# Kernel tuning notes

Hardware: AMD Instinct MI355X
Metric: run time of the kernel (lower is better)

Reference implementation:

```python
import jax, jax.numpy as jnp
import numpy as np

K = 10  # num_neighbors in original nn_index call


def setup_inputs() -> dict:
    key = jax.random.key(0)
    k1, k2, k3, k4 = jax.random.split(key, 4)
    B, OBS, ACT, N = 256, 32, 2, 500000
    obs = jax.random.normal(k1, (B, OBS), dtype=jnp.float32)
    action = jax.random.normal(k2, (B, ACT), dtype=jnp.float32)
    mem_sa = jax.random.normal(k3, (N, OBS + ACT), dtype=jnp.float32)
    mem_Q = jax.random.normal(k4, (N, 1), dtype=jnp.float32)
    return {"obs": obs, "action": action, "mem_sa": mem_sa, "mem_Q": mem_Q}


def reference(obs, action, mem_sa, mem_Q):
    # query: [B, D] state-action, brute-force kNN over memory table [N, D]
    q = jnp.concatenate([obs, action], axis=1)
    # squared Euclidean distances (FLANN returns squared L2): [B, N]
    d2 = (jnp.sum(q * q, axis=1, keepdims=True)
          - 2.0 * q @ mem_sa.T
          + jnp.sum(mem_sa * mem_sa, axis=1)[None, :])
    neg_d, idx = jax.lax.top_k(-d2, K)   # nearest K neighbors
    dists = -neg_d                        # [B, K], ascending
    Qs = mem_Q[idx, 0]                    # gather Q values: [B, K]
    # NOTE: original applies softmax to raw distances (not negated)
    weights = jax.nn.softmax(dists, axis=1)
    return jnp.sum(weights * Qs, axis=1)  # [B]
```

## Files before the change

### kernel.cpp

```cpp
#include <hip/hip_runtime.h>
#include <hip/hip_bf16.h>
#include <math.h>

#define NPTS   500000
#define NB     256
#define TOPK   10
#define CAP    2048
#define SBLK   1024
#define SPER   16
#define MARGIN 2.0f
#define NWCH   15625
#define FBLK   1536
#define LCAP   8
#define PMAIN  393216
#define OCAP   32768

typedef short v2s  __attribute__((ext_vector_type(2)));
typedef short v4s  __attribute__((ext_vector_type(4)));
typedef short v8s  __attribute__((ext_vector_type(8)));
typedef float v16f __attribute__((ext_vector_type(16)));

__device__ __forceinline__ unsigned short f2bf(float f) {
    unsigned u = __float_as_uint(f);
    unsigned r = u + 0x7FFFu + ((u >> 16) & 1u);
    return (unsigned short)(r >> 16);
}
__device__ __forceinline__ float bf2f(unsigned short h) {
    return __uint_as_float(((unsigned)h) << 16);
}
__device__ __forceinline__ v2s pk2(float2 f) {
    __hip_bfloat162 h = __float22bfloat162_rn(f);
    v2s r;
    __builtin_memcpy(&r, &h, 4);
    return r;
}

__device__ __forceinline__ float norm34(const float* __restrict__ r) {
    float a0 = 0.f, a1 = 0.f, a2 = 0.f, a3 = 0.f;
#pragma unroll
    for (int d = 0; d < 32; d += 4) {
        a0 = fmaf(r[d + 0], r[d + 0], a0);
        a1 = fmaf(r[d + 1], r[d + 1], a1);
        a2 = fmaf(r[d + 2], r[d + 2], a2);
        a3 = fmaf(r[d + 3], r[d + 3], a3);
    }
    a0 = fmaf(r[32], r[32], a0);
    a1 = fmaf(r[33], r[33], a1);
    return (a0 + a1) + (a2 + a3);
}
__device__ __forceinline__ float dot34(const float* __restrict__ r, const float* q) {
    float a0 = 0.f, a1 = 0.f, a2 = 0.f, a3 = 0.f;
#pragma unroll
    for (int d = 0; d < 32; d += 4) {
        a0 = fmaf(r[d + 0], q[d + 0], a0);
        a1 = fmaf(r[d + 1], q[d + 1], a1);
        a2 = fmaf(r[d + 2], q[d + 2], a2);
        a3 = fmaf(r[d + 3], q[d + 3], a3);
    }
    a0 = fmaf(r[32], q[32], a0);
    a1 = fmaf(r[33], q[33], a1);
    return (a0 + a1) + (a2 + a3);
}
__device__ __forceinline__ float dot34_v4(const float4* __restrict__ r4, const float* q) {
    float a0 = 0.f, a1 = 0.f, a2 = 0.f, a3 = 0.f;
#pragma unroll
    for (int dp = 0; dp < 8; ++dp) {
        float4 v = r4[dp];
        a0 = fmaf(v.x, q[4 * dp + 0], a0);
        a1 = fmaf(v.y, q[4 * dp + 1], a1);
        a2 = fmaf(v.z, q[4 * dp + 2], a2);
        a3 = fmaf(v.w, q[4 * dp + 3], a3);
    }
    float2 t = *(const float2*)(r4 + 8);
    a0 = fmaf(t.x, q[32], a0);
    a1 = fmaf(t.y, q[33], a1);
    return (a0 + a1) + (a2 + a3);
}
__device__ __forceinline__ void load_q(const float* __restrict__ obs,
                                       const float* __restrict__ act, int b, float* q) {
#pragma unroll
    for (int d = 0; d < 32; ++d) q[d] = obs[b * 32 + d];
    q[32] = act[b * 2 + 0];
    q[33] = act[b * 2 + 1];
}

__global__ __launch_bounds__(256, 4) void k_sample(const float* __restrict__ obs,
                                                   const float* __restrict__ act,
                                                   const float* __restrict__ msa,
                                                   float* __restrict__ minima) {
    __shared__ __align__(16) float sm[SPER * 36];
    __shared__ float smn[SPER];
    const int g = blockIdx.x, t = threadIdx.x;
    const int base = g * SPER;
    for (int i = t; i < SPER * 34; i += 256) {
        int row = i / 34, d = i - row * 34;
        sm[row * 36 + d] = msa[(size_t)base * 34 + i];
    }
    __syncthreads();
    if (t < SPER) smn[t] = norm34(&sm[t * 36]);
    __syncthreads();
    float q[34];
    load_q(obs, act, t, q);
    float best = __builtin_inff();
#pragma unroll
    for (int j = 0; j < SPER; ++j) {
        float s = fmaf(-2.f, dot34_v4((const float4*)&sm[j * 36], q), smn[j]);
        best = fminf(best, s);
    }
    minima[(size_t)t * SBLK + g] = best;
}

__global__ __launch_bounds__(64) void k_tau(const float* __restrict__ minima,
                                            const float* __restrict__ obs,
                                            const float* __restrict__ act,
                                            v8s* __restrict__ afrag,
                                            int* __restrict__ cursor) {
    __shared__ __align__(16) unsigned short qs[48];
    const int b = blockIdx.x, lane = threadIdx.x;
    if (b == 0 && lane == 0) { cursor[0] = 0; cursor[1] = 0; }
    float v[16];
#pragma unroll
    for (int k = 0; k < 16; ++k) v[k] = minima[(size_t)b * SBLK + lane + 64 * k];
    float last = 0.f;
    for (int r = 0; r < TOPK; ++r) {
        float lm = v[0]; int la = 0;
#pragma unroll
        for (int k = 1; k < 16; ++k) { if (v[k] < lm) { lm = v[k]; la = k; } }
        float wm = lm;
        for (int off = 32; off; off >>= 1) wm = fminf(wm, __shfl_xor(wm, off));
        unsigned long long msk = __ballot(lm == wm);
        int first = (int)__builtin_ctzll(msk);
        if (lane == first) {
#pragma unroll
            for (int k = 0; k < 16; ++k) { if (k == la) v[k] = __builtin_inff(); }
        }
        last = wm;
    }
    float val = 0.f;
    if (lane < 32)       val = obs[b * 32 + lane];
    else if (lane < 34)  val = act[b * 2 + (lane - 32)];
    else if (lane == 34) val = -0.5f;
    else if (lane == 35) val = 0.5f * (last + MARGIN);
    if (lane < 48) qs[lane] = (lane < 36) ? f2bf(val) : (unsigned short)0;
    __syncthreads();
    if (lane < 6) {
        int s = lane >> 1, half = lane & 1;
        int qt = b >> 5, mrow = b & 31;
        v8s frag = *(const v8s*)&qs[s * 16 + half * 8];
        afrag[(qt * 3 + s) * 64 + half * 32 + mrow] = frag;
    }
}

__global__ __launch_bounds__(256, 3) void k_filter(const float* __restrict__ msa,
                                                   const v8s* __restrict__ afrag,
                                                   int* __restrict__ cursor,
                                                   unsigned* __restrict__ pbuf,
                                                   int* __restrict__ posq) {
    __shared__ int lcount[NB];
    __shared__ int lcand[NB * LCAP];
    __shared__ int gbase;
    const int g = blockIdx.x, t = threadIdx.x;
    const int w = t >> 6, lane = t & 63;
    const int mrow = lane & 31, half = lane >> 5;
    lcount[t] = 0;
    __syncthreads();
    v8s A[8][3];
#pragma unroll
    for (int qt = 0; qt < 8; ++qt)
#pragma unroll
        for (int s = 0; s < 3; ++s)
            A[qt][s] = afrag[(qt * 3 + s) * 64 + lane];
    const v16f zacc = (v16f)0.0f;
    const int gw = g * 4 + w;
#pragma unroll 1
    for (int wc = gw; wc < NWCH; wc += FBLK * 4) {
        const int p0 = wc * 32 + mrow;
        const float* rp = msa + (size_t)p0 * 34;
        float2 e0 = *(const float2*)(rp + half * 8 + 0);
        float2 e1 = *(const float2*)(rp + half * 8 + 2);
        float2 e2 = *(const float2*)(rp + half * 8 + 4);
        float2 e3 = *(const float2*)(rp + half * 8 + 6);
        float2 e4 = *(const float2*)(rp + 16 + half * 8 + 0);
        float2 e5 = *(const float2*)(rp + 16 + half * 8 + 2);
        float2 e6 = *(const float2*)(rp + 16 + half * 8 + 4);
        float2 e7 = *(const float2*)(rp + 16 + half * 8 + 6);
        float2 e8 = *(const float2*)(rp + 32);
        float n0 = 0.f, n1 = 0.f;
        n0 = fmaf(e0.x, e0.x, n0); n1 = fmaf(e0.y, e0.y, n1);
        n0 = fmaf(e1.x, e1.x, n0); n1 = fmaf(e1.y, e1.y, n1);
        n0 = fmaf(e2.x, e2.x, n0); n1 = fmaf(e2.y, e2.y, n1);
        n0 = fmaf(e3.x, e3.x, n0); n1 = fmaf(e3.y, e3.y, n1);
        n0 = fmaf(e4.x, e4.x, n0); n1 = fmaf(e4.y, e4.y, n1);
        n0 = fmaf(e5.x, e5.x, n0); n1 = fmaf(e5.y, e5.y, n1);
        n0 = fmaf(e6.x, e6.x, n0); n1 = fmaf(e6.y, e6.y, n1);
        n0 = fmaf(e7.x, e7.x, n0); n1 = fmaf(e7.y, e7.y, n1);
        float part = n0 + n1;
        part = fmaf(e8.x, e8.x * 0.5f, part);
        part = fmaf(e8.y, e8.y * 0.5f, part);
        float nrm = part + __shfl_xor(part, 32);
        float thr = 0.5f * nrm;
        v4s b0lo = __builtin_shufflevector(pk2(e0), pk2(e1), 0, 1, 2, 3);
        v4s b0hi = __builtin_shufflevector(pk2(e2), pk2(e3), 0, 1, 2, 3);
        v8s B0 = __builtin_shufflevector(b0lo, b0hi, 0, 1, 2, 3, 4, 5, 6, 7);
        v4s b1lo = __builtin_shufflevector(pk2(e4), pk2(e5), 0, 1, 2, 3);
        v4s b1hi = __builtin_shufflevector(pk2(e6), pk2(e7), 0, 1, 2, 3);
        v8s B1 = __builtin_shufflevector(b1lo, b1hi, 0, 1, 2, 3, 4, 5, 6, 7);
        v8s B2 = (v8s)(short)0;
        if (half == 0) {
            v2s m33 = pk2(e8);
            B2[0] = m33[0];
            B2[1] = m33[1];
            B2[3] = (short)0x3F80;
        }
#pragma unroll
        for (int qt = 0; qt < 8; ++qt) {
            v16f acc = __builtin_amdgcn_mfma_f32_32x32x16_bf16(A[qt][0], B0, zacc, 0, 0, 0);
            acc = __builtin_amdgcn_mfma_f32_32x32x16_bf16(A[qt][1], B1, acc, 0, 0, 0);
            acc = __builtin_amdgcn_mfma_f32_32x32x16_bf16(A[qt][2], B2, acc, 0, 0, 0);
            unsigned hm = 0;
#pragma unroll
            for (int r = 0; r < 16; ++r) hm |= (acc[r] >= thr) ? (1u << r) : 0u;
            while (hm) {
                int r = __builtin_ctz(hm);
                hm &= hm - 1;
                int qq = qt * 32 + (r & 3) + 8 * (r >> 2) + 4 * half;
                int slot = atomicAdd(&lcount[qq], 1);
                if (slot < LCAP) lcand[qq * LCAP + slot] = p0;
                else {
                    int dg = atomicAdd(cursor + 1, 1);
                    if (dg < OCAP) pbuf[PMAIN + dg] = ((unsigned)qq << 19) | (unsigned)p0;
                }
            }
        }
    }
    __syncthreads();
    int n = lcount[t];
    if (n > LCAP) n = LCAP;
    lcount[t] = n;
    __syncthreads();
    for (int off = 1; off < 256; off <<= 1) {
        int v = (t >= off) ? lcount[t - off] : 0;
        __syncthreads();
        lcount[t] += v;
        __syncthreads();
    }
    int base_l = lcount[t] - n;
    if (t == 255) gbase = atomicAdd(cursor, lcount[255]);
    __syncthreads();
    int start = gbase + base_l;
    if (start >= PMAIN) { start = 0; n = 0; }
    else if (start + n > PMAIN) n = PMAIN - start;
    posq[g * NB + t] = start | (n << 20);
    for (int i = 0; i < n; ++i)
        pbuf[start + i] = (unsigned)lcand[t * LCAP + i];
}

__global__ __launch_bounds__(256) void k_final(const float* __restrict__ obs,
                                               const float* __restrict__ act,
                                               const float* __restrict__ msa,
                                               const unsigned* __restrict__ pbuf,
                                               const int* __restrict__ posq,
                                               const int* __restrict__ cursor,
                                               const float* __restrict__ memQ,
                                               float* __restrict__ out) {
    __shared__ float ls[CAP];
    __shared__ int   li[CAP];
    __shared__ int   sc[NB];
    __shared__ int   lcnt;
    __shared__ float rs[4];
    __shared__ int   ri[4];
    __shared__ float sel_s[TOPK];
    __shared__ int   sel_i[TOPK];
    const int b = blockIdx.x, t = threadIdx.x;
    const int lane = t & 63, wid = t >> 6;
    int nk[6], pk6[6], tot = 0;
#pragma unroll
    for (int k = 0; k < 6; ++k) {
        int packed = posq[(size_t)(t + 256 * k) * NB + b];
        nk[k] = (packed >> 20) & 0xF;
        pk6[k] = packed & 0xFFFFF;
        tot += nk[k];
    }
    sc[t] = tot;
    __syncthreads();
    for (int off = 1; off < 256; off <<= 1) {
        int v = (t >= off) ? sc[t - off] : 0;
        __syncthreads();
        sc[t] += v;
        __syncthreads();
    }
    int myoff = sc[t] - tot;
    if (t == 0) lcnt = (sc[255] > CAP) ? CAP : sc[255];
    __syncthreads();
#pragma unroll
    for (int k = 0; k < 6; ++k)
        for (int i = 0; i < nk[k]; ++i) {
            if (myoff < CAP) li[myoff] = (int)pbuf[pk6[k] + i];
            ++myoff;
        }
    int novf = cursor[1];
    if (novf > OCAP) novf = OCAP;
    for (int j = t; j < novf; j += 256) {
        unsigned pr = pbuf[PMAIN + j];
        if ((int)(pr >> 19) == b) {
            int s = atomicAdd(&lcnt, 1);
            if (s < CAP) li[s] = (int)(pr & 0x7FFFFu);
        }
    }
    __syncthreads();
    int cnt = lcnt;
    if (cnt > CAP) cnt = CAP;
    float q[34];
    load_q(obs, act, b, q);
    for (int j = t; j < cnt; j += 256) {
        const float* row = msa + (size_t)li[j] * 34;
        ls[j] = fmaf(-2.f, dot34(row, q), norm34(row));
    }
    __syncthreads();
    for (int k = 0; k < TOPK; ++k) {
        float bs = __builtin_inff();
        int   bi = 0x7fffffff;
        for (int j = t; j < cnt; j += 256) {
            float s = ls[j]; int i = li[j];
            if (s < bs || (s == bs && i < bi)) { bs = s; bi = i; }
        }
        for (int off = 32; off; off >>= 1) {
            float s2 = __shfl_down(bs, off);
            int   i2 = __shfl_down(bi, off);
            if (s2 < bs || (s2 == bs && i2 < bi)) { bs = s2; bi = i2; }
        }
        if (lane == 0) { rs[wid] = bs; ri[wid] = bi; }
        __syncthreads();
        if (t == 0) {
            float fs = rs[0]; int fi = ri[0];
#pragma unroll
            for (int ww = 1; ww < 4; ++ww) {
                if (rs[ww] < fs || (rs[ww] == fs && ri[ww] < fi)) { fs = rs[ww]; fi = ri[ww]; }
            }
            sel_s[k] = fs; sel_i[k] = fi;
        }
        __syncthreads();
        const int win = sel_i[k];
        for (int j = t; j < cnt; j += 256) {
            if (li[j] == win) ls[j] = __builtin_inff();
        }
        __syncthreads();
    }
    if (t == 0) {
        float m = sel_s[TOPK - 1];
        float wsum = 0.f, acc = 0.f;
#pragma unroll
        for (int k = 0; k < TOPK; ++k) {
            if (sel_i[k] == 0x7fffffff) continue;
            float w2 = expf(sel_s[k] - m);
            wsum += w2;
            acc = fmaf(w2, memQ[sel_i[k]], acc);
        }
        out[b] = acc / wsum;
    }
}

extern "C" void kernel_launch(void* const* d_in, const int* in_sizes, int n_in,
                              void* d_out, int out_size, void* d_ws, size_t ws_size,
                              hipStream_t stream) {
    const float* obs = (const float*)d_in[0];
    const float* act = (const float*)d_in[1];
    const float* msa = (const float*)d_in[2];
    const float* mq  = (const float*)d_in[3];
    float* out = (float*)d_out;

    char* ws = (char*)d_ws;
    int*      cursor = (int*)ws;
    v8s*      afrag  = (v8s*)(ws + 256);
    float*    minima = (float*)(ws + 32768);
    int*      posq   = (int*)(ws + 32768 + 1048576);
    unsigned* pbuf   = (unsigned*)(ws + 32768 + 1048576 + 1572864);

    k_sample<<<SBLK, 256, 0, stream>>>(obs, act, msa, minima);
    k_tau   <<<NB, 64, 0, stream>>>(minima, obs, act, afrag, cursor);
    k_filter<<<FBLK, 256, 0, stream>>>(msa, afrag, cursor, pbuf, posq);
    k_final <<<NB, 256, 0, stream>>>(obs, act, msa, pbuf, posq, cursor, mq, out);
}
```

Measured before the change: 174.9 us.

## Prefetch next memory rows in filter loop, cut filter grid, add max early-out

The filter kernel now software-pipelines its global loads, fetching the next chunk's rows into registers while MFMA and thresholding run on the current chunk. The grid shrinks from 1536 to 512 blocks, with launch bounds lowered to 2 waves per SIMD to make room for the extra registers, and the final kernel scans correspondingly fewer per-block segments. Each MFMA tile also gets a max-reduce early-out, so the per-row bitmask and atomics are skipped when no entry passes the threshold. The trade is more register pressure and lower occupancy in exchange for hidden load latency and less divergent per-tile work.

```diff
diff --git a/kernel.cpp b/kernel.cpp
--- a/kernel.cpp
+++ b/kernel.cpp
@@ -10,7 +10,8 @@
 #define SPER   16
 #define MARGIN 2.0f
 #define NWCH   15625
-#define FBLK   1536
+#define FBLK   512
+#define NSEG   2
 #define LCAP   8
 #define PMAIN  393216
 #define OCAP   32768
@@ -82,6 +83,18 @@
     for (int d = 0; d < 32; ++d) q[d] = obs[b * 32 + d];
     q[32] = act[b * 2 + 0];
     q[33] = act[b * 2 + 1];
+}
+__device__ __forceinline__ void load9(float2* __restrict__ e,
+                                      const float* __restrict__ rp, int half) {
+    e[0] = *(const float2*)(rp + half * 8 + 0);
+    e[1] = *(const float2*)(rp + half * 8 + 2);
+    e[2] = *(const float2*)(rp + half * 8 + 4);
+    e[3] = *(const float2*)(rp + half * 8 + 6);
+    e[4] = *(const float2*)(rp + 16 + half * 8 + 0);
+    e[5] = *(const float2*)(rp + 16 + half * 8 + 2);
+    e[6] = *(const float2*)(rp + 16 + half * 8 + 4);
+    e[7] = *(const float2*)(rp + 16 + half * 8 + 6);
+    e[8] = *(const float2*)(rp + 32);
 }
 
 __global__ __launch_bounds__(256, 4) void k_sample(const float* __restrict__ obs,
@@ -151,7 +164,7 @@
     }
 }
 
-__global__ __launch_bounds__(256, 3) void k_filter(const float* __restrict__ msa,
+__global__ __launch_bounds__(256, 2) void k_filter(const float* __restrict__ msa,
                                                    const v8s* __restrict__ afrag,
                                                    int* __restrict__ cursor,
                                                    unsigned* __restrict__ pbuf,
@@ -162,52 +175,49 @@
     const int g = blockIdx.x, t = threadIdx.x;
     const int w = t >> 6, lane = t & 63;
     const int mrow = lane & 31, half = lane >> 5;
-    lcount[t] = 0;
-    __syncthreads();
     v8s A[8][3];
 #pragma unroll
     for (int qt = 0; qt < 8; ++qt)
 #pragma unroll
         for (int s = 0; s < 3; ++s)
             A[qt][s] = afrag[(qt * 3 + s) * 64 + lane];
+    lcount[t] = 0;
+    __syncthreads();
     const v16f zacc = (v16f)0.0f;
     const int gw = g * 4 + w;
+    const int step = FBLK * 4;
+    float2 c[9], nx[9];
+    int wc = gw;
+    load9(c, msa + (size_t)(wc * 32 + mrow) * 34, half);
 #pragma unroll 1
-    for (int wc = gw; wc < NWCH; wc += FBLK * 4) {
+    for (; wc < NWCH; ) {
+        const int wn = wc + step;
+        const int pn = (wn < NWCH) ? wn : gw;
+        load9(nx, msa + (size_t)(pn * 32 + mrow) * 34, half);
         const int p0 = wc * 32 + mrow;
-        const float* rp = msa + (size_t)p0 * 34;
-        float2 e0 = *(const float2*)(rp + half * 8 + 0);
-        float2 e1 = *(const float2*)(rp + half * 8 + 2);
-        float2 e2 = *(const float2*)(rp + half * 8 + 4);
-        float2 e3 = *(const float2*)(rp + half * 8 + 6);
-        float2 e4 = *(const float2*)(rp + 16 + half * 8 + 0);
-        float2 e5 = *(const float2*)(rp + 16 + half * 8 + 2);
-        float2 e6 = *(const float2*)(rp + 16 + half * 8 + 4);
-        float2 e7 = *(const float2*)(rp + 16 + half * 8 + 6);
-        float2 e8 = *(const float2*)(rp + 32);
         float n0 = 0.f, n1 = 0.f;
-        n0 = fmaf(e0.x, e0.x, n0); n1 = fmaf(e0.y, e0.y, n1);
-        n0 = fmaf(e1.x, e1.x, n0); n1 = fmaf(e1.y, e1.y, n1);
-        n0 = fmaf(e2.x, e2.x, n0); n1 = fmaf(e2.y, e2.y, n1);
-        n0 = fmaf(e3.x, e3.x, n0); n1 = fmaf(e3.y, e3.y, n1);
-        n0 = fmaf(e4.x, e4.x, n0); n1 = fmaf(e4.y, e4.y, n1);
-        n0 = fmaf(e5.x, e5.x, n0); n1 = fmaf(e5.y, e5.y, n1);
-        n0 = fmaf(e6.x, e6.x, n0); n1 = fmaf(e6.y, e6.y, n1);
-        n0 = fmaf(e7.x, e7.x, n0); n1 = fmaf(e7.y, e7.y, n1);
+        n0 = fmaf(c[0].x, c[0].x, n0); n1 = fmaf(c[0].y, c[0].y, n1);
+        n0 = fmaf(c[1].x, c[1].x, n0); n1 = fmaf(c[1].y, c[1].y, n1);
+        n0 = fmaf(c[2].x, c[2].x, n0); n1 = fmaf(c[2].y, c[2].y, n1);
+        n0 = fmaf(c[3].x, c[3].x, n0); n1 = fmaf(c[3].y, c[3].y, n1);
+        n0 = fmaf(c[4].x, c[4].x, n0); n1 = fmaf(c[4].y, c[4].y, n1);
+        n0 = fmaf(c[5].x, c[5].x, n0); n1 = fmaf(c[5].y, c[5].y, n1);
+        n0 = fmaf(c[6].x, c[6].x, n0); n1 = fmaf(c[6].y, c[6].y, n1);
+        n0 = fmaf(c[7].x, c[7].x, n0); n1 = fmaf(c[7].y, c[7].y, n1);
         float part = n0 + n1;
-        part = fmaf(e8.x, e8.x * 0.5f, part);
-        part = fmaf(e8.y, e8.y * 0.5f, part);
+        part = fmaf(c[8].x, c[8].x * 0.5f, part);
+        part = fmaf(c[8].y, c[8].y * 0.5f, part);
         float nrm = part + __shfl_xor(part, 32);
         float thr = 0.5f * nrm;
-        v4s b0lo = __builtin_shufflevector(pk2(e0), pk2(e1), 0, 1, 2, 3);
-        v4s b0hi = __builtin_shufflevector(pk2(e2), pk2(e3), 0, 1, 2, 3);
+        v4s b0lo = __builtin_shufflevector(pk2(c[0]), pk2(c[1]), 0, 1, 2, 3);
+        v4s b0hi = __builtin_shufflevector(pk2(c[2]), pk2(c[3]), 0, 1, 2, 3);
         v8s B0 = __builtin_shufflevector(b0lo, b0hi, 0, 1, 2, 3, 4, 5, 6, 7);
-        v4s b1lo = __builtin_shufflevector(pk2(e4), pk2(e5), 0, 1, 2, 3);
-        v4s b1hi = __builtin_shufflevector(pk2(e6), pk2(e7), 0, 1, 2, 3);
+        v4s b1lo = __builtin_shufflevector(pk2(c[4]), pk2(c[5]), 0, 1, 2, 3);
+        v4s b1hi = __builtin_shufflevector(pk2(c[6]), pk2(c[7]), 0, 1, 2, 3);
         v8s B1 = __builtin_shufflevector(b1lo, b1hi, 0, 1, 2, 3, 4, 5, 6, 7);
         v8s B2 = (v8s)(short)0;
         if (half == 0) {
-            v2s m33 = pk2(e8);
+            v2s m33 = pk2(c[8]);
             B2[0] = m33[0];
             B2[1] = m33[1];
             B2[3] = (short)0x3F80;
@@ -217,21 +227,32 @@
             v16f acc = __builtin_amdgcn_mfma_f32_32x32x16_bf16(A[qt][0], B0, zacc, 0, 0, 0);
             acc = __builtin_amdgcn_mfma_f32_32x32x16_bf16(A[qt][1], B1, acc, 0, 0, 0);
             acc = __builtin_amdgcn_mfma_f32_32x32x16_bf16(A[qt][2], B2, acc, 0, 0, 0);
-            unsigned hm = 0;
-#pragma unroll
-            for (int r = 0; r < 16; ++r) hm |= (acc[r] >= thr) ? (1u << r) : 0u;
-            while (hm) {
-                int r = __builtin_ctz(hm);
-                hm &= hm - 1;
-                int qq = qt * 32 + (r & 3) + 8 * (r >> 2) + 4 * half;
-                int slot = atomicAdd(&lcount[qq], 1);
-                if (slot < LCAP) lcand[qq * LCAP + slot] = p0;
-                else {
-                    int dg = atomicAdd(cursor + 1, 1);
-                    if (dg < OCAP) pbuf[PMAIN + dg] = ((unsigned)qq << 19) | (unsigned)p0;
+            float m01 = fmaxf(acc[0], acc[1]),   m23 = fmaxf(acc[2], acc[3]);
+            float m45 = fmaxf(acc[4], acc[5]),   m67 = fmaxf(acc[6], acc[7]);
+            float m89 = fmaxf(acc[8], acc[9]),   mab = fmaxf(acc[10], acc[11]);
+            float mcd = fmaxf(acc[12], acc[13]), mef = fmaxf(acc[14], acc[15]);
+            float mx = fmaxf(fmaxf(fmaxf(m01, m23), fmaxf(m45, m67)),
+                             fmaxf(fmaxf(m89, mab), fmaxf(mcd, mef)));
+            if (mx >= thr) {
+                unsigned hm = 0;
+#pragma unroll
+                for (int r = 0; r < 16; ++r) hm |= (acc[r] >= thr) ? (1u << r) : 0u;
+                while (hm) {
+                    int r = __builtin_ctz(hm);
+                    hm &= hm - 1;
+                    int qq = qt * 32 + (r & 3) + 8 * (r >> 2) + 4 * half;
+                    int slot = atomicAdd(&lcount[qq], 1);
+                    if (slot < LCAP) lcand[qq * LCAP + slot] = p0;
+                    else {
+                        int dg = atomicAdd(cursor + 1, 1);
+                        if (dg < OCAP) pbuf[PMAIN + dg] = ((unsigned)qq << 19) | (unsigned)p0;
+                    }
                 }
             }
         }
+#pragma unroll
+        for (int i = 0; i < 9; ++i) c[i] = nx[i];
+        wc = wn;
     }
     __syncthreads();
     int n = lcount[t];
@@ -273,9 +294,9 @@
     __shared__ int   sel_i[TOPK];
     const int b = blockIdx.x, t = threadIdx.x;
     const int lane = t & 63, wid = t >> 6;
-    int nk[6], pk6[6], tot = 0;
-#pragma unroll
-    for (int k = 0; k < 6; ++k) {
+    int nk[NSEG], pk6[NSEG], tot = 0;
+#pragma unroll
+    for (int k = 0; k < NSEG; ++k) {
         int packed = posq[(size_t)(t + 256 * k) * NB + b];
         nk[k] = (packed >> 20) & 0xF;
         pk6[k] = packed & 0xFFFFF;
@@ -293,7 +314,7 @@
     if (t == 0) lcnt = (sc[255] > CAP) ? CAP : sc[255];
     __syncthreads();
 #pragma unroll
-    for (int k = 0; k < 6; ++k)
+    for (int k = 0; k < NSEG; ++k)
         for (int i = 0; i < nk[k]; ++i) {
             if (myoff < CAP) li[myoff] = (int)pbuf[pk6[k] + i];
             ++myoff;
```

Result: faster. 171.3 us (-2.1%).

## Stage memory chunks through double-buffered LDS and split query tiles across waves

Applied to the files above, without the earlier changes.

The filter kernel now loads each 32-point chunk of the memory table cooperatively into a double-buffered shared-memory tile, prefetching the next chunk while the current one is processed. Each of the four waves handles two of the eight query tiles for the same chunk, so each wave holds fewer A fragments and occupancy rises. A cheap max-reduction skips building the hit mask when no accumulator passes the threshold. The block count drops to 1024, and the final kernel reads 4 position segments instead of 6 to match. The trade-off is an added __syncthreads per chunk and 4 waves each recomputing norms and bf16 packing for the same points.

```diff
diff --git a/kernel.cpp b/kernel.cpp
--- a/kernel.cpp
+++ b/kernel.cpp
@@ -10,10 +10,12 @@
 #define SPER   16
 #define MARGIN 2.0f
 #define NWCH   15625
-#define FBLK   1536
+#define FBLK   1024
+#define NSEG   4
 #define LCAP   8
 #define PMAIN  393216
 #define OCAP   32768
+#define CHB    4352
 
 typedef short v2s  __attribute__((ext_vector_type(2)));
 typedef short v4s  __attribute__((ext_vector_type(4)));
@@ -151,31 +153,41 @@
     }
 }
 
-__global__ __launch_bounds__(256, 3) void k_filter(const float* __restrict__ msa,
+__global__ __launch_bounds__(256, 4) void k_filter(const float* __restrict__ msa,
                                                    const v8s* __restrict__ afrag,
                                                    int* __restrict__ cursor,
                                                    unsigned* __restrict__ pbuf,
                                                    int* __restrict__ posq) {
+    __shared__ __align__(16) float chunk[2][CHB / 4];
     __shared__ int lcount[NB];
     __shared__ int lcand[NB * LCAP];
     __shared__ int gbase;
     const int g = blockIdx.x, t = threadIdx.x;
     const int w = t >> 6, lane = t & 63;
     const int mrow = lane & 31, half = lane >> 5;
+    v8s A[2][3];
+#pragma unroll
+    for (int j = 0; j < 2; ++j)
+#pragma unroll
+        for (int s = 0; s < 3; ++s)
+            A[j][s] = afrag[((w * 2 + j) * 3 + s) * 64 + lane];
     lcount[t] = 0;
-    __syncthreads();
-    v8s A[8][3];
-#pragma unroll
-    for (int qt = 0; qt < 8; ++qt)
-#pragma unroll
-        for (int s = 0; s < 3; ++s)
-            A[qt][s] = afrag[(qt * 3 + s) * 64 + lane];
     const v16f zacc = (v16f)0.0f;
-    const int gw = g * 4 + w;
-#pragma unroll 1
-    for (int wc = gw; wc < NWCH; wc += FBLK * 4) {
-        const int p0 = wc * 32 + mrow;
-        const float* rp = msa + (size_t)p0 * 34;
+
+    float4 sreg; float treg = 0.f;
+    const char* mb = (const char*)msa;
+    auto stage_load = [&](int c) {
+        const char* cb = mb + (size_t)c * CHB;
+        sreg = *(const float4*)(cb + t * 16);
+        if (t < 64) treg = *(const float*)(cb + 4096 + t * 4);
+    };
+    auto stage_write = [&](int nb) {
+        *(float4*)((char*)&chunk[nb][0] + t * 16) = sreg;
+        if (t < 64) *(float*)((char*)&chunk[nb][0] + 4096 + t * 4) = treg;
+    };
+    auto process = [&](int cur, int c) {
+        const float* rp = &chunk[cur][0] + mrow * 34;
+        const int p0 = c * 32 + mrow;
         float2 e0 = *(const float2*)(rp + half * 8 + 0);
         float2 e1 = *(const float2*)(rp + half * 8 + 2);
         float2 e2 = *(const float2*)(rp + half * 8 + 4);
@@ -213,25 +225,54 @@
             B2[3] = (short)0x3F80;
         }
 #pragma unroll
-        for (int qt = 0; qt < 8; ++qt) {
-            v16f acc = __builtin_amdgcn_mfma_f32_32x32x16_bf16(A[qt][0], B0, zacc, 0, 0, 0);
-            acc = __builtin_amdgcn_mfma_f32_32x32x16_bf16(A[qt][1], B1, acc, 0, 0, 0);
-            acc = __builtin_amdgcn_mfma_f32_32x32x16_bf16(A[qt][2], B2, acc, 0, 0, 0);
-            unsigned hm = 0;
-#pragma unroll
-            for (int r = 0; r < 16; ++r) hm |= (acc[r] >= thr) ? (1u << r) : 0u;
-            while (hm) {
-                int r = __builtin_ctz(hm);
-                hm &= hm - 1;
-                int qq = qt * 32 + (r & 3) + 8 * (r >> 2) + 4 * half;
-                int slot = atomicAdd(&lcount[qq], 1);
-                if (slot < LCAP) lcand[qq * LCAP + slot] = p0;
-                else {
-                    int dg = atomicAdd(cursor + 1, 1);
-                    if (dg < OCAP) pbuf[PMAIN + dg] = ((unsigned)qq << 19) | (unsigned)p0;
+        for (int j = 0; j < 2; ++j) {
+            const int qt = w * 2 + j;
+            v16f acc = __builtin_amdgcn_mfma_f32_32x32x16_bf16(A[j][0], B0, zacc, 0, 0, 0);
+            acc = __builtin_amdgcn_mfma_f32_32x32x16_bf16(A[j][1], B1, acc, 0, 0, 0);
+            acc = __builtin_amdgcn_mfma_f32_32x32x16_bf16(A[j][2], B2, acc, 0, 0, 0);
+            float m0 = fmaxf(fmaxf(acc[0], acc[1]), acc[2]);
+            float m1 = fmaxf(fmaxf(acc[3], acc[4]), acc[5]);
+            float m2 = fmaxf(fmaxf(acc[6], acc[7]), acc[8]);
+            float m3 = fmaxf(fmaxf(acc[9], acc[10]), acc[11]);
+            float m4 = fmaxf(fmaxf(acc[12], acc[13]), acc[14]);
+            float mx = fmaxf(fmaxf(fmaxf(m0, m1), m2),
+                             fmaxf(fmaxf(m3, m4), acc[15]));
+            if (mx >= thr) {
+                unsigned hm = 0;
+#pragma unroll
+                for (int r = 0; r < 16; ++r) hm |= (acc[r] >= thr) ? (1u << r) : 0u;
+                while (hm) {
+                    int r = __builtin_ctz(hm);
+                    hm &= hm - 1;
+                    int qq = qt * 32 + (r & 3) + 8 * (r >> 2) + 4 * half;
+                    int slot = atomicAdd(&lcount[qq], 1);
+                    if (slot < LCAP) lcand[qq * LCAP + slot] = p0;
+                    else {
+                        int dg = atomicAdd(cursor + 1, 1);
+                        if (dg < OCAP) pbuf[PMAIN + dg] = ((unsigned)qq << 19) | (unsigned)p0;
+                    }
                 }
             }
         }
+    };
+
+    int c = g;
+    stage_load(c);
+    stage_write(0);
+    __syncthreads();
+    int cur = 0;
+#pragma unroll 1
+    for (;;) {
+        const int cn = c + FBLK;
+        const bool hn = (cn < NWCH);
+        if (hn) stage_load(cn);
+        __builtin_amdgcn_sched_barrier(0);
+        process(cur, c);
+        if (!hn) break;
+        stage_write(cur ^ 1);
+        __syncthreads();
+        cur ^= 1;
+        c = cn;
     }
     __syncthreads();
     int n = lcount[t];
@@ -273,9 +314,9 @@
     __shared__ int   sel_i[TOPK];
     const int b = blockIdx.x, t = threadIdx.x;
     const int lane = t & 63, wid = t >> 6;
-    int nk[6], pk6[6], tot = 0;
-#pragma unroll
-    for (int k = 0; k < 6; ++k) {
+    int nk[NSEG], pk6[NSEG], tot = 0;
+#pragma unroll
+    for (int k = 0; k < NSEG; ++k) {
         int packed = posq[(size_t)(t + 256 * k) * NB + b];
         nk[k] = (packed >> 20) & 0xF;
         pk6[k] = packed & 0xFFFFF;
@@ -293,7 +334,7 @@
     if (t == 0) lcnt = (sc[255] > CAP) ? CAP : sc[255];
     __syncthreads();
 #pragma unroll
-    for (int k = 0; k < 6; ++k)
+    for (int k = 0; k < NSEG; ++k)
         for (int i = 0; i < nk[k]; ++i) {
             if (myoff < CAP) li[myoff] = (int)pbuf[pk6[k] + i];
             ++myoff;
```

Measured after the change: 171.6 us. Within noise of the previous version (-1.9%).
